# Kernel optimization log

Measured on AMD Instinct MI355X. Metric: run time of the kernel, lower is better.

## Reference

```python
import jax, jax.numpy as jnp
import numpy as np

CLAMP = 6.0  # clamp_delta


def _causal_dw_conv(x, w, b):
    # x: [B, D, L], w: [D, W] depthwise taps, b: [D]; torch Conv1d(groups=D, padding=W-1)[..., :L]
    W = w.shape[1]
    L = x.shape[-1]
    xp = jnp.pad(x, ((0, 0), (0, 0), (W - 1, 0)))
    y = b[None, :, None]
    for i in range(W):  # small fixed kernel width (2 or 4)
        y = y + xp[:, :, i:i + L] * w[:, i][None, :, None]
    return y


def _selective_scan(u, delta, A, Bm, Cm, D, z, delta_bias):
    # u, delta: [B, Di, L]; A: [Di, N]; Bm, Cm: [B, N, L]; D, delta_bias: [Di]; z: [B, Di, L]
    d = jax.nn.softplus(delta + delta_bias[None, :, None])

    def step(s, inp):
        d_t, b_t, c_t, u_t = inp  # [B,Di], [B,N], [B,N], [B,Di]
        s = s * jnp.exp(d_t[..., None] * A) + (d_t * u_t)[..., None] * b_t[:, None, :]
        return s, jnp.einsum('bdn,bn->bd', s, c_t)

    s0 = jnp.zeros((u.shape[0], A.shape[0], A.shape[1]), u.dtype)
    xs = (d.transpose(2, 0, 1), Bm.transpose(2, 0, 1), Cm.transpose(2, 0, 1), u.transpose(2, 0, 1))
    _, ys = jax.lax.scan(step, s0, xs)  # ys: [L, B, Di]
    y = ys.transpose(1, 2, 0) + D[:, None] * u
    return y * jax.nn.silu(z)


def _mamba(h, in_w, conv_w, conv_b, xproj_w, dt_w, dt_b, A_log, D, out_w):
    # standard Mamba block (no fast path), expand=1: h [B, L, dm] -> [B, L, dm]
    xz = jnp.einsum('bld,ed->bel', h, in_w)
    x, z = jnp.split(xz, 2, axis=1)
    x = jax.nn.silu(_causal_dw_conv(x, conv_w, conv_b))
    xdbl = jnp.einsum('bdl,ed->ble', x, xproj_w)
    r = dt_w.shape[1]
    n = A_log.shape[1]
    dt, Bm, Cm = jnp.split(xdbl, [r, r + n], axis=-1)
    delta = jnp.einsum('blr,dr->bdl', dt, dt_w)  # bias added inside scan as delta_bias
    y = _selective_scan(x, delta, -jnp.exp(A_log), Bm.transpose(0, 2, 1), Cm.transpose(0, 2, 1), D, z, dt_b)
    return jnp.einsum('bdl,ed->ble', y, out_w)


def setup_inputs() -> dict:
    rng = np.random.default_rng(0)
    dm, ds, dc, di, r = 1024, 16, 4, 2048, 64  # d_model, d_state, d_conv, d_inner, dt_rank
    mdm, mds, mdc, mr = 64, 4, 2, 4            # inner dt-Mamba dims (expand=1)
    B, L = 2, 1024

    def g(*s, std=0.02):
        return jnp.asarray(rng.standard_normal(s).astype(np.float32) * std)

    def inv_dt(d, lo=1e-3, hi=0.1):
        dt = np.exp(rng.uniform(size=d) * (np.log(hi) - np.log(lo)) + np.log(lo)).clip(min=1e-4)
        return jnp.asarray((dt + np.log(-np.expm1(-dt))).astype(np.float32))

    return dict(
        hidden_states=g(B, L, dm, std=1.0),
        in_proj_w=g(2 * di, dm),
        conv_w=g(di, dc, std=0.2),
        conv_b=g(di, std=0.02),
        x_proj_w=g(r + 2 * ds, di),
        dt_out_w=g(di, r, std=0.01),
        dt_out_b=inv_dt(di),
        A_log=jnp.log(jnp.tile(jnp.arange(1, ds + 1, dtype=jnp.float32), (di, 1))),
        D=jnp.ones(di, jnp.float32),
        out_proj_w=g(dm, di),
        m_in_w=g(2 * mdm, mdm),
        m_conv_w=g(mdm, mdc, std=0.3),
        m_conv_b=g(mdm, std=0.02),
        m_xproj_w=g(mr + 2 * mds, mdm),
        m_dt_w=g(mdm, mr, std=0.5),
        m_dt_b=inv_dt(mdm),
        m_A_log=jnp.log(jnp.tile(jnp.arange(1, mds + 1, dtype=jnp.float32), (mdm, 1))),
        m_D=jnp.ones(mdm, jnp.float32),
        m_out_w=g(mdm, mdm),
    )


def reference(hidden_states, in_proj_w, conv_w, conv_b, x_proj_w, dt_out_w, dt_out_b,
              A_log, D, out_proj_w, m_in_w, m_conv_w, m_conv_b, m_xproj_w, m_dt_w,
              m_dt_b, m_A_log, m_D, m_out_w):
    r = m_in_w.shape[1]  # dt_rank == inner d_model
    n = A_log.shape[1]   # d_state
    # in_proj (no bias): [B, 2*Di, L]
    xz = jnp.einsum('bld,ed->bel', hidden_states, in_proj_w)
    x, z = jnp.split(xz, 2, axis=1)
    x = jax.nn.silu(_causal_dw_conv(x, conv_w, conv_b))
    xdbl = jnp.einsum('bdl,ed->ble', x, x_proj_w)  # [B, L, r + 2n]
    dt_in, Bm, Cm = jnp.split(xdbl, [r, r + n], axis=-1)
    # nested dt-Mamba computes delta
    dt_m = _mamba(dt_in, m_in_w, m_conv_w, m_conv_b, m_xproj_w, m_dt_w, m_dt_b, m_A_log, m_D, m_out_w)
    delta = jnp.einsum('blr,dr->bld', dt_m, dt_out_w) + dt_out_b
    delta = jnp.clip(delta, -CLAMP, CLAMP).transpose(0, 2, 1)  # [B, Di, L]
    y = _selective_scan(x, delta, -jnp.exp(A_log), Bm.transpose(0, 2, 1), Cm.transpose(0, 2, 1),
                        D, z, dt_out_b)
    return jnp.einsum('bdl,ed->ble', y, out_proj_w)
```

## Files before the change

### kernel.cpp

```cpp
#include <hip/hip_runtime.h>
#include <hip/hip_bf16.h>

#define DEVFN __device__ __forceinline__

DEVFN float siluf(float x)     { return x / (1.f + __expf(-x)); }
DEVFN float softplusf(float x) { return fmaxf(x, 0.f) + log1pf(__expf(-fabsf(x))); }

DEVFN ushort f2bf(float f) {
    __bf16 h = (__bf16)f;
    return __builtin_bit_cast(ushort, h);
}

template<int CTRL>
DEVFN float dpp_addf(float x) {
    union { float f; int i; } a, r;
    a.f = x;
    r.i = __builtin_amdgcn_update_dpp(0, a.i, CTRL, 0xF, 0xF, true);
    return x + r.f;
}
DEVFN float sum16(float p) {
    p = dpp_addf<0x128>(p);
    p = dpp_addf<0x124>(p);
    p = dpp_addf<0x4E>(p);
    p = dpp_addf<0xB1>(p);
    return p;
}
DEVFN float sum4(float p) {
    p = dpp_addf<0x4E>(p);
    p = dpp_addf<0xB1>(p);
    return p;
}

typedef __bf16 bf16x8 __attribute__((ext_vector_type(8)));
typedef float  f32x4  __attribute__((ext_vector_type(4)));
typedef ushort us8    __attribute__((ext_vector_type(8)));

template<int BM, int BN, bool A_F32, bool B_F32>
__global__ __launch_bounds__(256) void mfma_gemm_nt(
    const void* __restrict__ Av, const void* __restrict__ Bv,
    float* __restrict__ C, int M, int N, int K,
    long long Abs, long long Bbs, long long Cbs)
{
    constexpr int MFR = BM / 32;
    constexpr int NFR = BN / 32;
    __shared__ __align__(16) ushort As[BM][40];
    __shared__ __align__(16) ushort Bs[BN][40];

    const int tid = threadIdx.x;
    const int gx = gridDim.x, gy = gridDim.y;
    const int orig = (blockIdx.z * gy + blockIdx.y) * gx + blockIdx.x;
    const int cpx = (gx * gy * gridDim.z) >> 3;
    const int swz = (orig & 7) * cpx + (orig >> 3);
    const int bx = swz % gx;
    const int byz = swz / gx;
    const int by = byz % gy;
    const int b  = byz / gy;
    const int m0 = bx * BM;
    const int n0 = by * BN;
    const int lane = tid & 63;
    const int wid  = tid >> 6;
    const int wr   = wid >> 1;
    const int wc   = wid & 1;
    const int fr   = lane & 15;
    const int kq   = lane >> 4;

    f32x4 acc[MFR][NFR];
    #pragma unroll
    for (int i = 0; i < MFR; ++i)
        #pragma unroll
        for (int j = 0; j < NFR; ++j)
            acc[i][j] = (f32x4){0.f, 0.f, 0.f, 0.f};

    const int arow = tid >> 1;
    const int kh   = (tid & 1) * 16;

    for (int kt = 0; kt < K; kt += 32) {
        if (kt) __syncthreads();
        if (BM == 128 || arow < BM) {
            const long long off = (long long)b * Abs + (long long)(m0 + arow) * K + kt + kh;
            us8 lo, hi;
            if (A_F32) {
                const float4* p = (const float4*)((const float*)Av + off);
                float4 v0 = p[0], v1 = p[1], v2 = p[2], v3 = p[3];
                lo = (us8){f2bf(v0.x), f2bf(v0.y), f2bf(v0.z), f2bf(v0.w),
                           f2bf(v1.x), f2bf(v1.y), f2bf(v1.z), f2bf(v1.w)};
                hi = (us8){f2bf(v2.x), f2bf(v2.y), f2bf(v2.z), f2bf(v2.w),
                           f2bf(v3.x), f2bf(v3.y), f2bf(v3.z), f2bf(v3.w)};
            } else {
                const us8* p = (const us8*)((const ushort*)Av + off);
                lo = p[0]; hi = p[1];
            }
            *(us8*)&As[arow][kh]     = lo;
            *(us8*)&As[arow][kh + 8] = hi;
        }
        if (BN == 128 || arow < BN) {
            const long long off = (long long)b * Bbs + (long long)(n0 + arow) * K + kt + kh;
            us8 lo, hi;
            if (B_F32) {
                const float4* p = (const float4*)((const float*)Bv + off);
                float4 v0 = p[0], v1 = p[1], v2 = p[2], v3 = p[3];
                lo = (us8){f2bf(v0.x), f2bf(v0.y), f2bf(v0.z), f2bf(v0.w),
                           f2bf(v1.x), f2bf(v1.y), f2bf(v1.z), f2bf(v1.w)};
                hi = (us8){f2bf(v2.x), f2bf(v2.y), f2bf(v2.z), f2bf(v2.w),
                           f2bf(v3.x), f2bf(v3.y), f2bf(v3.z), f2bf(v3.w)};
            } else {
                const us8* p = (const us8*)((const ushort*)Bv + off);
                lo = p[0]; hi = p[1];
            }
            *(us8*)&Bs[arow][kh]     = lo;
            *(us8*)&Bs[arow][kh + 8] = hi;
        }
        __syncthreads();

        bf16x8 af[MFR], bfv[NFR];
        #pragma unroll
        for (int mi = 0; mi < MFR; ++mi)
            af[mi] = *(const bf16x8*)&As[wr * (BM / 2) + mi * 16 + fr][kq * 8];
        #pragma unroll
        for (int ni = 0; ni < NFR; ++ni)
            bfv[ni] = *(const bf16x8*)&Bs[wc * (BN / 2) + ni * 16 + fr][kq * 8];
        #pragma unroll
        for (int mi = 0; mi < MFR; ++mi)
            #pragma unroll
            for (int ni = 0; ni < NFR; ++ni)
                acc[mi][ni] = __builtin_amdgcn_mfma_f32_16x16x32_bf16(
                    af[mi], bfv[ni], acc[mi][ni], 0, 0, 0);
    }

    #pragma unroll
    for (int mi = 0; mi < MFR; ++mi) {
        const int gm = m0 + wr * (BM / 2) + mi * 16 + kq * 4;
        #pragma unroll
        for (int ni = 0; ni < NFR; ++ni) {
            const int gn = n0 + wc * (BN / 2) + ni * 16 + fr;
            f32x4 v = acc[mi][ni];
            #pragma unroll
            for (int r = 0; r < 4; ++r)
                C[(long long)b * Cbs + (long long)(gm + r) * N + gn] = v[r];
        }
    }
}

__global__ __launch_bounds__(256) void transpose_gate_f32_bf16(
    const float* __restrict__ p, const float* __restrict__ u,
    const float* __restrict__ z, const float* __restrict__ Dp,
    ushort* __restrict__ yt, int D, int Lx,
    long long Pbs, long long Ubs)
{
    __shared__ float ts[32][33];
    const int l0 = blockIdx.x * 32, d0 = blockIdx.y * 32, b = blockIdx.z;
    const int tx = threadIdx.x & 31, ty = threadIdx.x >> 5;
    const float* pb = p + (size_t)b * Pbs + (size_t)d0 * Lx + l0;
    const float* ub = u + (size_t)b * Ubs + (size_t)d0 * Lx + l0;
    const float* zb = z + (size_t)b * Pbs + (size_t)d0 * Lx + l0;
    #pragma unroll
    for (int r = ty; r < 32; r += 8) {
        float Dd = Dp[d0 + r];
        float pv = pb[(size_t)r * Lx + tx];
        float uv = ub[(size_t)r * Lx + tx];
        float zv = zb[(size_t)r * Lx + tx];
        ts[r][tx] = (pv + Dd * uv) * siluf(zv);
    }
    __syncthreads();
    ushort* ytb = yt + ((size_t)b * Lx + l0) * D + d0;
    #pragma unroll
    for (int r = ty; r < 32; r += 8)
        ytb[(size_t)r * D + tx] = f2bf(ts[tx][r]);
}

template<bool BKC, bool OUTM, bool CLIP, bool BIAS>
__global__ __launch_bounds__(256) void gemm_kernel(
    const float* __restrict__ A, const float* __restrict__ X,
    const float* __restrict__ bias, float* __restrict__ C,
    int M, int N, int K, int Xld, long long Xbs, long long Cbs)
{
    __shared__ __align__(16) float As[16][68];
    __shared__ __align__(16) float Xs[16][68];
    const int m0 = blockIdx.x * 64;
    const int n0 = blockIdx.y * 64;
    const int b  = blockIdx.z;
    const float* Xb = X + (long long)b * Xbs;
    const int tid = threadIdx.x;
    const int te = tid & 15, tl = tid >> 4;
    float acc[4][4] = {};

    for (int k0 = 0; k0 < K; k0 += 16) {
        #pragma unroll
        for (int idx = tid; idx < 1024; idx += 256) {
            int e = idx >> 4, kk = idx & 15;
            int m = m0 + e, k = k0 + kk;
            As[kk][e] = (m < M && k < K) ? A[(long long)m * K + k] : 0.f;
        }
        if (BKC) {
            #pragma unroll
            for (int idx = tid; idx < 1024; idx += 256) {
                int n = idx >> 4, kk = idx & 15;
                int nn = n0 + n, k = k0 + kk;
                Xs[kk][n] = (nn < N && k < K) ? Xb[(long long)nn * Xld + k] : 0.f;
            }
        } else {
            #pragma unroll
            for (int idx = tid; idx < 1024; idx += 256) {
                int kk = idx >> 6, n = idx & 63;
                int nn = n0 + n, k = k0 + kk;
                Xs[kk][n] = (nn < N && k < K) ? Xb[(long long)k * Xld + nn] : 0.f;
            }
        }
        __syncthreads();
        #pragma unroll
        for (int kk = 0; kk < 16; ++kk) {
            float4 a4 = *reinterpret_cast<const float4*>(&As[kk][te * 4]);
            float4 x4 = *reinterpret_cast<const float4*>(&Xs[kk][tl * 4]);
            float av[4] = {a4.x, a4.y, a4.z, a4.w};
            float xv[4] = {x4.x, x4.y, x4.z, x4.w};
            #pragma unroll
            for (int i = 0; i < 4; ++i)
                #pragma unroll
                for (int j = 0; j < 4; ++j)
                    acc[i][j] += av[i] * xv[j];
        }
        __syncthreads();
    }

    #pragma unroll
    for (int i = 0; i < 4; ++i) {
        int m = m0 + te * 4 + i;
        if (m >= M) continue;
        float bv = BIAS ? bias[m] : 0.f;
        #pragma unroll
        for (int j = 0; j < 4; ++j) {
            int n = n0 + tl * 4 + j;
            if (n >= N) continue;
            float v = acc[i][j] + bv;
            if (CLIP) v = fminf(fmaxf(v, -6.f), 6.f);
            if (OUTM) C[(long long)b * Cbs + (long long)m * N + n] = v;
            else      C[(long long)b * Cbs + (long long)n * M + m] = v;
        }
    }
}

__global__ __launch_bounds__(256) void xprojT_splitk(
    const float* __restrict__ W, const float* __restrict__ X,
    float* __restrict__ P, int L, int K, int KS)
{
    __shared__ float Xs[16][68];
    __shared__ float Ws[16][100];
    const int l0 = blockIdx.x * 64;
    const int ks = blockIdx.y;
    const int b  = blockIdx.z;
    const int Kc = K / KS;
    const int tid = threadIdx.x;
    const int tl = (tid & 15) * 4;
    const int te = (tid >> 4) * 6;
    float acc[4][6] = {};
    const float* Xb = X + (size_t)b * K * L;

    for (int d0 = ks * Kc; d0 < (ks + 1) * Kc; d0 += 16) {
        #pragma unroll
        for (int o = tid; o < 1024; o += 256) {
            int dd = o >> 6, l = o & 63;
            Xs[dd][l] = Xb[(size_t)(d0 + dd) * L + l0 + l];
        }
        #pragma unroll
        for (int o = tid; o < 1536; o += 256) {
            int e = o >> 4, dd = o & 15;
            Ws[dd][e] = W[(size_t)e * K + d0 + dd];
        }
        __syncthreads();
        #pragma unroll
        for (int dd = 0; dd < 16; ++dd) {
            float4 x4 = *(const float4*)&Xs[dd][tl];
            float xv[4] = {x4.x, x4.y, x4.z, x4.w};
            float wv[6];
            #pragma unroll
            for (int j = 0; j < 6; ++j) wv[j] = Ws[dd][te + j];
            #pragma unroll
            for (int i = 0; i < 4; ++i)
                #pragma unroll
                for (int j = 0; j < 6; ++j)
                    acc[i][j] += xv[i] * wv[j];
        }
        __syncthreads();
    }

    float* Pz = P + ((size_t)(b * KS + ks) * L + l0) * 96;
    #pragma unroll
    for (int i = 0; i < 4; ++i)
        #pragma unroll
        for (int j = 0; j < 6; ++j)
            Pz[(size_t)(tl + i) * 96 + te + j] = acc[i][j];
}

__global__ __launch_bounds__(256) void reduce_splitk(
    const float* __restrict__ P, float* __restrict__ C, int slab, int KS)
{
    const int i4 = blockIdx.x * 256 + threadIdx.x;
    const int b  = blockIdx.y;
    if (i4 * 4 >= slab) return;
    const float* base = P + (size_t)b * KS * slab + (size_t)i4 * 4;
    float4 acc = make_float4(0.f, 0.f, 0.f, 0.f);
    for (int ks = 0; ks < KS; ++ks) {
        float4 v = *(const float4*)(base + (size_t)ks * slab);
        acc.x += v.x; acc.y += v.y; acc.z += v.z; acc.w += v.w;
    }
    *(float4*)(C + (size_t)b * slab + (size_t)i4 * 4) = acc;
}

__global__ __launch_bounds__(256) void conv4_silu_kernel(
    const float* __restrict__ in, const float* __restrict__ w,
    const float* __restrict__ bias, float* __restrict__ out,
    int B, int D, int L, int IC)
{
    int idx = blockIdx.x * 256 + threadIdx.x;
    int nL4 = L >> 2;
    if (idx >= B * D * nL4) return;
    int l4 = (idx % nL4) * 4;
    int d  = (idx / nL4) % D;
    int b  = idx / (nL4 * D);
    const float* xp = in + ((size_t)b * IC + d) * L;
    float4 cur = *(const float4*)(xp + l4);
    float4 prev = make_float4(0.f, 0.f, 0.f, 0.f);
    if (l4) prev = *(const float4*)(xp + l4 - 4);
    const float4 wv = *(const float4*)(w + d * 4);
    float bv = bias[d];
    float y0 = bv + wv.x*prev.y + wv.y*prev.z + wv.z*prev.w + wv.w*cur.x;
    float y1 = bv + wv.x*prev.z + wv.y*prev.w + wv.z*cur.x  + wv.w*cur.y;
    float y2 = bv + wv.x*prev.w + wv.y*cur.x  + wv.z*cur.y  + wv.w*cur.z;
    float y3 = bv + wv.x*cur.x  + wv.y*cur.y  + wv.z*cur.z  + wv.w*cur.w;
    *(float4*)(out + ((size_t)b * D + d) * L + l4) =
        make_float4(siluf(y0), siluf(y1), siluf(y2), siluf(y3));
}

__global__ __launch_bounds__(256) void inner_xproj_dt_conv_kernel(
    const float* __restrict__ mxz, const float* __restrict__ cw,
    const float* __restrict__ cb, const float* __restrict__ xw,
    const float* __restrict__ dtw, float* __restrict__ mxconv,
    float* __restrict__ mxdblT, float* __restrict__ mdelta, int L)
{
    __shared__ float xs[64][65];
    __shared__ float xwl[12][64];
    __shared__ float dtl[64][4];
    __shared__ float xd[4][65];
    const int tid = threadIdx.x;
    const int l0 = blockIdx.x * 64;
    const int b  = blockIdx.y;

    {
        const int k = tid >> 2, seg = (tid & 3) * 16;
        const float* xp = mxz + ((size_t)b * 128 + k) * L + l0 + seg;
        float prevv = (l0 + seg > 0) ? xp[-1] : 0.f;
        float4 v0 = *(const float4*)(xp);
        float4 v1 = *(const float4*)(xp + 4);
        float4 v2 = *(const float4*)(xp + 8);
        float4 v3 = *(const float4*)(xp + 12);
        float vals[16] = {v0.x, v0.y, v0.z, v0.w, v1.x, v1.y, v1.z, v1.w,
                          v2.x, v2.y, v2.z, v2.w, v3.x, v3.y, v3.z, v3.w};
        const float w0 = cw[k * 2], w1 = cw[k * 2 + 1], bv = cb[k];
        float outv[16];
        #pragma unroll
        for (int t = 0; t < 16; ++t) {
            outv[t] = siluf(w0 * prevv + w1 * vals[t] + bv);
            prevv = vals[t];
        }
        #pragma unroll
        for (int t = 0; t < 16; ++t) xs[k][seg + t] = outv[t];
        float* op = mxconv + ((size_t)b * 64 + k) * L + l0 + seg;
        *(float4*)(op)      = make_float4(outv[0], outv[1], outv[2], outv[3]);
        *(float4*)(op + 4)  = make_float4(outv[4], outv[5], outv[6], outv[7]);
        *(float4*)(op + 8)  = make_float4(outv[8], outv[9], outv[10], outv[11]);
        *(float4*)(op + 12) = make_float4(outv[12], outv[13], outv[14], outv[15]);
    }
    if (tid < 768) xwl[tid / 64][tid % 64] = xw[tid];
    dtl[tid >> 2][tid & 3] = dtw[tid];
    __syncthreads();

    for (int o = tid; o < 768; o += 256) {
        int e = o >> 6, l = o & 63;
        float acc = 0.f;
        #pragma unroll
        for (int k = 0; k < 64; ++k) acc += xwl[e][k] * xs[k][l];
        mxdblT[((size_t)b * L + l0 + l) * 12 + e] = acc;
        if (e < 4) xd[e][l] = acc;
    }
    __syncthreads();

    for (int o = tid; o < 4096; o += 256) {
        int dch = o >> 6, l = o & 63;
        float acc = dtl[dch][0] * xd[0][l] + dtl[dch][1] * xd[1][l]
                  + dtl[dch][2] * xd[2][l] + dtl[dch][3] * xd[3][l];
        mdelta[((size_t)b * 64 + dch) * L + l0 + l] = acc;
    }
}

__global__ __launch_bounds__(256) void outproj_dt_kernel(
    const float* __restrict__ ym, const float* __restrict__ mow,
    const float* __restrict__ dtw, const float* __restrict__ dtb,
    float* __restrict__ delta, int L, int Dch)
{
    __shared__ float xs[64][68];
    __shared__ float ws[64][64];
    __shared__ float dts[64][68];
    __shared__ float As[16][68];
    const int tid = threadIdx.x;
    const int l0 = blockIdx.x * 64;
    const int m0 = blockIdx.y * 64;
    const int b  = blockIdx.z;

    for (int o = tid; o < 4096; o += 256) {
        int k = o >> 6, l = o & 63;
        xs[k][l] = ym[((size_t)b * 64 + k) * L + l0 + l];
        ws[k][l] = mow[o];
    }
    __syncthreads();

    for (int o = tid; o < 4096; o += 256) {
        int e = o >> 6, l = o & 63;
        float acc = 0.f;
        #pragma unroll
        for (int k = 0; k < 64; ++k) acc += ws[e][k] * xs[k][l];
        dts[e][l] = acc;
    }

    const int te = tid & 15, tl = tid >> 4;
    float acc[4][4] = {};
    for (int k0 = 0; k0 < 64; k0 += 16) {
        __syncthreads();
        for (int idx = tid; idx < 1024; idx += 256) {
            int e = idx >> 6, m = idx & 63;
            As[e][m] = dtw[(size_t)(m0 + m) * 64 + k0 + e];
        }
        __syncthreads();
        #pragma unroll
        for (int kk = 0; kk < 16; ++kk) {
            float4 a4 = *(const float4*)&As[kk][te * 4];
            float4 x4 = *(const float4*)&dts[k0 + kk][tl * 4];
            float av[4] = {a4.x, a4.y, a4.z, a4.w};
            float xv[4] = {x4.x, x4.y, x4.z, x4.w};
            #pragma unroll
            for (int i = 0; i < 4; ++i)
                #pragma unroll
                for (int j = 0; j < 4; ++j)
                    acc[i][j] += av[i] * xv[j];
        }
    }

    #pragma unroll
    for (int i = 0; i < 4; ++i) {
        int m = m0 + te * 4 + i;
        float bv = dtb[m];
        #pragma unroll
        for (int j = 0; j < 4; ++j) {
            float v = fminf(fmaxf(acc[i][j] + bv, -6.f), 6.f);
            delta[((size_t)b * Dch + m) * L + l0 + tl * 4 + j] = v;
        }
    }
}

__global__ __launch_bounds__(512) void scan_outer8_kernel(
    const float* __restrict__ delta, const float* __restrict__ u,
    const float* __restrict__ xdblT, const float* __restrict__ A_log,
    const float* __restrict__ dt_bias, float* __restrict__ y,
    int Dch, int L, long long Ybs)
{
    __shared__ float2 dtdu[32][34];
    __shared__ float2 PS[16][33];

    const int tid = threadIdx.x;
    const int b = blockIdx.y;
    const int d = blockIdx.x;
    const size_t rbase = ((size_t)b * Dch + d) * L;

    {
        const int l0 = tid * 2;
        float2 d2 = *(const float2*)(delta + rbase + l0);
        float2 u2 = *(const float2*)(u + rbase + l0);
        float bias = dt_bias[d];
        float dv[2] = {d2.x, d2.y};
        float uv[2] = {u2.x, u2.y};
        #pragma unroll
        for (int t = 0; t < 2; ++t) {
            float dt = softplusf(dv[t] + bias);
            dtdu[l0 >> 5][(l0 & 31) + t] = make_float2(dt, dt * uv[t]);
        }
    }
    __syncthreads();

    const int c = tid >> 4;
    const int n = tid & 15;
    const float Adn = -__expf(A_log[d * 16 + n]);
    const float* brow = xdblT + ((size_t)b * L + (size_t)c * 32) * 96 + 64 + n;

    float s = 0.f, sumdt = 0.f;
    for (int q = 0; q < 8; ++q) {
        #pragma unroll
        for (int t = 0; t < 4; ++t) {
            int l = q * 4 + t;
            float bv = brow[(size_t)l * 96];
            float2 dd = dtdu[c][l];
            float a = __expf(dd.x * Adn);
            s = fmaf(a, s, dd.y * bv);
            sumdt += dd.x;
        }
    }
    PS[n][c] = make_float2(__expf(sumdt * Adn), s);
    __syncthreads();

    float s0 = 0.f;
    for (int j = 0; j < c; ++j) {
        float2 ps = PS[n][j];
        s0 = fmaf(ps.x, s0, ps.y);
    }

    {
        const size_t ybase = (size_t)b * Ybs + (size_t)d * L + (size_t)c * 32;
        float s2 = s0;
        for (int q = 0; q < 8; ++q) {
            float yv[4];
            #pragma unroll
            for (int t = 0; t < 4; ++t) {
                int l = q * 4 + t;
                float bv = brow[(size_t)l * 96];
                float cv = brow[(size_t)l * 96 + 16];
                float2 dd = dtdu[c][l];
                float a = __expf(dd.x * Adn);
                s2 = fmaf(a, s2, dd.y * bv);
                yv[t] = sum16(s2 * cv);
            }
            if (n == 0)
                *(float4*)(y + ybase + q * 4) = make_float4(yv[0], yv[1], yv[2], yv[3]);
        }
    }
}

__global__ __launch_bounds__(256) void scan_inner6_kernel(
    const float* __restrict__ mdelta, const float* __restrict__ mu,
    const float* __restrict__ mxz, const float* __restrict__ mxdblT,
    const float* __restrict__ mA_log, const float* __restrict__ mDp,
    const float* __restrict__ mdt_b, float* __restrict__ ym, int L)
{
    __shared__ __align__(16) float2 dtdu[64][18];
    __shared__ float2 PS[4][66];

    const int tid = threadIdx.x;
    const int b = blockIdx.y;
    const int d = blockIdx.x;
    const size_t base = ((size_t)b * 64 + d) * L;

    {
        const int l0 = tid * 4;
        float4 d4 = *(const float4*)(mdelta + base + l0);
        float4 u4 = *(const float4*)(mu + base + l0);
        float bias = mdt_b[d];
        float dv[4] = {d4.x, d4.y, d4.z, d4.w};
        float uv[4] = {u4.x, u4.y, u4.z, u4.w};
        #pragma unroll
        for (int t = 0; t < 4; ++t) {
            float dt = softplusf(dv[t] + bias);
            dtdu[tid >> 2][(tid & 3) * 4 + t] = make_float2(dt, dt * uv[t]);
        }
    }
    __syncthreads();

    const int c = tid >> 2;
    const int n = tid & 3;
    const float Adn = -__expf(mA_log[d * 4 + n]);
    const float* brow = mxdblT + ((size_t)b * L + (size_t)c * 16) * 12 + 4 + n;

    float s = 0.f, sumdt = 0.f;
    for (int q = 0; q < 4; ++q) {
        float4 dA = *(const float4*)&dtdu[c][q * 4];
        float4 dB = *(const float4*)&dtdu[c][q * 4 + 2];
        float dt_[4] = {dA.x, dA.z, dB.x, dB.z};
        float du_[4] = {dA.y, dA.w, dB.y, dB.w};
        #pragma unroll
        for (int t = 0; t < 4; ++t) {
            float bv = brow[(size_t)(q * 4 + t) * 12];
            float a = __expf(dt_[t] * Adn);
            s = fmaf(a, s, du_[t] * bv);
            sumdt += dt_[t];
        }
    }
    PS[n][c] = make_float2(__expf(sumdt * Adn), s);
    __syncthreads();

    float s0 = 0.f;
    for (int j = 0; j < c; ++j) {
        float2 ps = PS[n][j];
        s0 = fmaf(ps.x, s0, ps.y);
    }

    {
        const float* up = mu + base + c * 16;
        const float* zp = mxz + ((size_t)b * 128 + 64 + d) * L + c * 16;
        const float Dd = mDp[d];
        float s2 = s0;
        for (int q = 0; q < 4; ++q) {
            float4 dA = *(const float4*)&dtdu[c][q * 4];
            float4 dB = *(const float4*)&dtdu[c][q * 4 + 2];
            float dt_[4] = {dA.x, dA.z, dB.x, dB.z};
            float du_[4] = {dA.y, dA.w, dB.y, dB.w};
            float4 u4 = *(const float4*)(up + q * 4);
            float4 z4 = *(const float4*)(zp + q * 4);
            float uv[4] = {u4.x, u4.y, u4.z, u4.w};
            float zv[4] = {z4.x, z4.y, z4.z, z4.w};
            float yv[4];
            #pragma unroll
            for (int t = 0; t < 4; ++t) {
                int l = q * 4 + t;
                float bv = brow[(size_t)l * 12];
                float cv = brow[(size_t)l * 12 + 4];
                float a = __expf(dt_[t] * Adn);
                s2 = fmaf(a, s2, du_[t] * bv);
                float p = sum4(s2 * cv);
                yv[t] = (p + Dd * uv[t]) * siluf(zv[t]);
            }
            if (n == 0)
                *(float4*)(ym + base + c * 16 + q * 4) = make_float4(yv[0], yv[1], yv[2], yv[3]);
        }
    }
}

extern "C" void kernel_launch(void* const* d_in, const int* in_sizes, int n_in,
                              void* d_out, int out_size, void* d_ws, size_t ws_size,
                              hipStream_t stream)
{
    const float* h         = (const float*)d_in[0];
    const float* in_w      = (const float*)d_in[1];
    const float* conv_w    = (const float*)d_in[2];
    const float* conv_b    = (const float*)d_in[3];
    const float* xproj_w   = (const float*)d_in[4];
    const float* dt_out_w  = (const float*)d_in[5];
    const float* dt_out_b  = (const float*)d_in[6];
    const float* A_log     = (const float*)d_in[7];
    const float* Dp        = (const float*)d_in[8];
    const float* out_w     = (const float*)d_in[9];
    const float* m_in_w    = (const float*)d_in[10];
    const float* m_conv_w  = (const float*)d_in[11];
    const float* m_conv_b  = (const float*)d_in[12];
    const float* m_xproj_w = (const float*)d_in[13];
    const float* m_dt_w    = (const float*)d_in[14];
    const float* m_dt_b    = (const float*)d_in[15];
    const float* m_A_log   = (const float*)d_in[16];
    const float* m_Dp      = (const float*)d_in[17];
    const float* m_out_w   = (const float*)d_in[18];
    float* out = (float*)d_out;

    const int B = 2, L = 1024, dm = 1024, di = 2048;

    float* ws     = (float*)d_ws;
    float* xz     = ws;
    float* xconv  = xz     + (size_t)B * 2 * di * L;
    float* xdblT  = xconv  + (size_t)B * di * L;
    float* mxz    = xdblT  + (size_t)B * 96 * L;
    float* mxconv = mxz    + (size_t)B * 128 * L;
    float* mxdblT = mxconv + (size_t)B * 64 * L;
    float* mdelta = mxdblT + (size_t)B * 12 * L;
    float* ym     = mdelta + (size_t)B * 64 * L;
    float* dtm    = ym     + (size_t)B * 64 * L;
    float* delta  = dtm    + (size_t)B * 64 * L;
    ushort* yt    = (ushort*)delta;
    float* part   = delta;

    dim3 blk(256);

    mfma_gemm_nt<128, 128, true, true><<<dim3(4096 / 128, L / 128, B), blk, 0, stream>>>(
        in_w, h, xz, 2 * di, L, dm, 0LL, (long long)L * dm, (long long)2 * di * L);

    {
        int total = B * di * (L / 4);
        conv4_silu_kernel<<<dim3((total + 255) / 256), blk, 0, stream>>>(
            xz, conv_w, conv_b, xconv, B, di, L, 2 * di);
    }

    {
        const int KS = 16;
        xprojT_splitk<<<dim3(L / 64, KS, B), blk, 0, stream>>>(
            xproj_w, xconv, part, L, di, KS);
        int slab = 96 * L;
        reduce_splitk<<<dim3((slab / 4 + 255) / 256, B), blk, 0, stream>>>(
            part, xdblT, slab, KS);
    }

    gemm_kernel<true, true, false, false><<<dim3(2, 16, B), blk, 0, stream>>>(
        m_in_w, xdblT, nullptr, mxz, 128, L, 64, 96, (long long)96 * L, (long long)128 * L);

    inner_xproj_dt_conv_kernel<<<dim3(L / 64, B), blk, 0, stream>>>(
        mxz, m_conv_w, m_conv_b, m_xproj_w, m_dt_w, mxconv, mxdblT, mdelta, L);

    scan_inner6_kernel<<<dim3(64, B), blk, 0, stream>>>(
        mdelta, mxconv, mxz, mxdblT, m_A_log, m_Dp, m_dt_b, ym, L);

    outproj_dt_kernel<<<dim3(L / 64, di / 64, B), blk, 0, stream>>>(
        ym, m_out_w, dt_out_w, dt_out_b, delta, L, di);

    scan_outer8_kernel<<<dim3(di, B), dim3(512), 0, stream>>>(
        delta, xconv, xdblT, A_log, dt_out_b, xz, di, L, (long long)2 * di * L);

    transpose_gate_f32_bf16<<<dim3(L / 32, di / 32, B), blk, 0, stream>>>(
        xz, xconv, xz + (size_t)di * L, Dp, yt, di, L,
        (long long)2 * di * L, (long long)di * L);

    mfma_gemm_nt<64, 64, false, true><<<dim3(B * L / 64, dm / 64, 1), blk, 0, stream>>>(
        yt, out_w, out, B * L, dm, di, 0LL, 0LL, 0LL);
}
```

Baseline: 254.6 us.

## Split-K the output projection GEMM with swizzled block order and reduction

```diff
diff --git a/kernel.cpp b/kernel.cpp
--- a/kernel.cpp
+++ b/kernel.cpp
@@ -137,6 +137,92 @@
             #pragma unroll
             for (int r = 0; r < 4; ++r)
                 C[(long long)b * Cbs + (long long)(gm + r) * N + gn] = v[r];
+        }
+    }
+}
+
+__global__ __launch_bounds__(256) void mfma_gemm_nt_sk(
+    const ushort* __restrict__ Av, const float* __restrict__ Bv,
+    float* __restrict__ P, int M, int N, int K, int KS)
+{
+    constexpr int BM = 64, BN = 64;
+    __shared__ __align__(16) ushort As[BM][40];
+    __shared__ __align__(16) ushort Bs[BN][40];
+
+    const int tid = threadIdx.x;
+    const int gx = gridDim.x, gy = gridDim.y;
+    const int orig = (blockIdx.z * gy + blockIdx.y) * gx + blockIdx.x;
+    const int cpx = (gx * gy * gridDim.z) >> 3;
+    const int swz = (orig & 7) * cpx + (orig >> 3);
+    const int bx = swz % gx;
+    const int byz = swz / gx;
+    const int by = byz % gy;
+    const int ks = byz / gy;
+    const int m0 = bx * BM;
+    const int n0 = by * BN;
+    const int Kc = K / KS;
+    const int lane = tid & 63;
+    const int wid  = tid >> 6;
+    const int wr   = wid >> 1;
+    const int wc   = wid & 1;
+    const int fr   = lane & 15;
+    const int kq   = lane >> 4;
+
+    f32x4 acc[2][2];
+    #pragma unroll
+    for (int i = 0; i < 2; ++i)
+        #pragma unroll
+        for (int j = 0; j < 2; ++j)
+            acc[i][j] = (f32x4){0.f, 0.f, 0.f, 0.f};
+
+    const int arow = tid >> 1;
+    const int kh   = (tid & 1) * 16;
+
+    for (int kt = ks * Kc; kt < (ks + 1) * Kc; kt += 32) {
+        if (kt != ks * Kc) __syncthreads();
+        if (arow < BM) {
+            const us8* p = (const us8*)(Av + (long long)(m0 + arow) * K + kt + kh);
+            *(us8*)&As[arow][kh]     = p[0];
+            *(us8*)&As[arow][kh + 8] = p[1];
+        } else {
+            const int brow = arow - BM;
+            const float4* p = (const float4*)(Bv + (long long)(n0 + brow) * K + kt + kh);
+            float4 v0 = p[0], v1 = p[1], v2 = p[2], v3 = p[3];
+            us8 lo = (us8){f2bf(v0.x), f2bf(v0.y), f2bf(v0.z), f2bf(v0.w),
+                           f2bf(v1.x), f2bf(v1.y), f2bf(v1.z), f2bf(v1.w)};
+            us8 hi = (us8){f2bf(v2.x), f2bf(v2.y), f2bf(v2.z), f2bf(v2.w),
+                           f2bf(v3.x), f2bf(v3.y), f2bf(v3.z), f2bf(v3.w)};
+            *(us8*)&Bs[brow][kh]     = lo;
+            *(us8*)&Bs[brow][kh + 8] = hi;
+        }
+        __syncthreads();
+
+        bf16x8 af[2], bfv[2];
+        #pragma unroll
+        for (int mi = 0; mi < 2; ++mi)
+            af[mi] = *(const bf16x8*)&As[wr * 32 + mi * 16 + fr][kq * 8];
+        #pragma unroll
+        for (int ni = 0; ni < 2; ++ni)
+            bfv[ni] = *(const bf16x8*)&Bs[wc * 32 + ni * 16 + fr][kq * 8];
+        #pragma unroll
+        for (int mi = 0; mi < 2; ++mi)
+            #pragma unroll
+            for (int ni = 0; ni < 2; ++ni)
+                acc[mi][ni] = __builtin_amdgcn_mfma_f32_16x16x32_bf16(
+                    af[mi], bfv[ni], acc[mi][ni], 0, 0, 0);
+    }
+
+    float* Pz = P + (long long)ks * M * N;
+    #pragma unroll
+    for (int mi = 0; mi < 2; ++mi) {
+        const int gm = m0 + wr * 32 + mi * 16 + kq * 4;
+        #pragma unroll
+        for (int ni = 0; ni < 2; ++ni) {
+            const int gn = n0 + wc * 32 + ni * 16 + fr;
+            f32x4 v = acc[mi][ni];
+            #pragma unroll
+            for (int r = 0; r < 4; ++r)
+                Pz[(long long)(gm + r) * N + gn] = v[r];
         }
     }
 }
@@ -700,6 +786,13 @@
         xz, xconv, xz + (size_t)di * L, Dp, yt, di, L,
         (long long)2 * di * L, (long long)di * L);
 
-    mfma_gemm_nt<64, 64, false, true><<<dim3(B * L / 64, dm / 64, 1), blk, 0, stream>>>(
-        yt, out_w, out, B * L, dm, di, 0LL, 0LL, 0LL);
-}
+    {
+        const int KS = 4;
+        float* gpart = xz;
+        mfma_gemm_nt_sk<<<dim3(B * L / 64, dm / 64, KS), blk, 0, stream>>>(
+            yt, out_w, gpart, B * L, dm, di, KS);
+        int slab = B * L * dm;
+        reduce_splitk<<<dim3((slab / 4 + 255) / 256, 1), blk, 0, stream>>>(
+            gpart, out, slab, KS);
+    }
+}
```

Result: faster. 245.1 us (-3.7%).
